# Optimization experiments

Measured on AMD Instinct MI355X. Metric: run time of the kernel, lower is better.

The kernel has to match this reference:

```python
import jax, jax.numpy as jnp
import numpy as np

N = 30000      # num_nodes
E = 480000     # num_edges
NF = 128       # node_features
EF = 64        # edge_features
HID = 256      # hidden_dim
L = 4          # num_layers
H = 8          # heads
D = HID // H   # per-head dim = 32
SCALE = 0.02


def _ln(x, g, b, eps=1e-5):
    m = x.mean(-1, keepdims=True)
    v = ((x - m) ** 2).mean(-1, keepdims=True)
    return (x - m) * jax.lax.rsqrt(v + eps) * g + b


def _mlp_head(x, W1, b1, W2, b2):
    return jax.nn.sigmoid(jax.nn.relu(x @ W1 + b1) @ W2 + b2)


def setup_inputs() -> dict:
    key = jax.random.key(0)
    ks = jax.random.split(key, 32)
    r = lambda k, shp: SCALE * jax.random.normal(k, shp, dtype=jnp.float32)
    inp = {
        'x': jax.random.normal(ks[0], (N, NF), dtype=jnp.float32),
        'edge_attr': jax.random.normal(ks[1], (E, EF), dtype=jnp.float32),
        'edge_index': jax.random.randint(ks[2], (2, E), 0, N, dtype=jnp.int32),
        # encoders
        'enc_Wn': r(ks[3], (NF, HID)), 'enc_bn': jnp.zeros((HID,), jnp.float32),
        'enc_We': r(ks[4], (EF, HID)), 'enc_be': jnp.zeros((HID,), jnp.float32),
        # stacked TransformerConv params for L layers
        'Wq': r(ks[5], (L, HID, HID)), 'bq': jnp.zeros((L, HID), jnp.float32),
        'Wk': r(ks[6], (L, HID, HID)), 'bk': jnp.zeros((L, HID), jnp.float32),
        'Wv': r(ks[7], (L, HID, HID)), 'bv': jnp.zeros((L, HID), jnp.float32),
        'We': r(ks[8], (L, HID, HID)),  # lin_edge has no bias in PyG
        'Wsk': r(ks[9], (L, HID, HID)), 'bsk': jnp.zeros((L, HID), jnp.float32),
        # shared LayerNorm (module reuses self.norm every layer)
        'ln_g': jnp.ones((HID,), jnp.float32), 'ln_b': jnp.zeros((HID,), jnp.float32),
        # contagion predictor
        'cp_W1': r(ks[10], (HID, HID // 2)), 'cp_b1': jnp.zeros((HID // 2,), jnp.float32),
        'cp_W2': r(ks[11], (HID // 2, 1)), 'cp_b2': jnp.zeros((1,), jnp.float32),
        # systemic risk predictor
        'sp_W1': r(ks[12], (HID, HID // 2)), 'sp_b1': jnp.zeros((HID // 2,), jnp.float32),
        'sp_W2': r(ks[13], (HID // 2, 1)), 'sp_b2': jnp.zeros((1,), jnp.float32),
    }
    return inp


def reference(x, edge_attr, edge_index, enc_Wn, enc_bn, enc_We, enc_be,
              Wq, bq, Wk, bk, Wv, bv, We, Wsk, bsk, ln_g, ln_b,
              cp_W1, cp_b1, cp_W2, cp_b2, sp_W1, sp_b1, sp_W2, sp_b2):
    src, dst = edge_index[0], edge_index[1]
    h = x @ enc_Wn + enc_bn                 # [N,HID]
    e = edge_attr @ enc_We + enc_be         # [E,HID]
    inv_sqrt_d = 1.0 / jnp.sqrt(jnp.asarray(D, h.dtype))
    for l in range(L):
        # TransformerConv: query at dst, key/value at src, edge bias on both k and v
        q = (h @ Wq[l] + bq[l]).reshape(N, H, D)[dst]            # [E,H,D]
        ke = (e @ We[l]).reshape(E, H, D)                        # [E,H,D]
        k = (h @ Wk[l] + bk[l]).reshape(N, H, D)[src] + ke
        v = (h @ Wv[l] + bv[l]).reshape(N, H, D)[src] + ke
        score = (q * k).sum(-1) * inv_sqrt_d                     # [E,H]
        smax = jax.ops.segment_max(score, dst, num_segments=N)   # [N,H]
        p = jnp.exp(score - smax[dst])
        denom = jax.ops.segment_sum(p, dst, num_segments=N)
        alpha = p / (denom[dst] + 1e-16)                         # scatter-softmax
        agg = jax.ops.segment_sum(alpha[..., None] * v, dst, num_segments=N)
        out = agg.reshape(N, HID) + h @ Wsk[l] + bsk[l]          # concat heads + root skip
        h = _ln(h + out, ln_g, ln_b)                             # residual + shared LN (eval: no dropout)
    g = h.mean(0, keepdims=True)                                 # [1,HID] global mean pool
    contagion_risk = _mlp_head(h, cp_W1, cp_b1, cp_W2, cp_b2)    # [N,1]
    systemic_risk = _mlp_head(g, sp_W1, sp_b1, sp_W2, sp_b2)     # [1,1]
    return h, g, contagion_risk, systemic_risk
```

## Files before the change

### kernel.cpp

```cpp
#include <hip/hip_runtime.h>
#include <cstddef>
#include <cstdint>

#define NN 30000
#define EE 480000
#define NFD 128
#define EFD 64
#define HID 256
#define NL 4
#define NH 8

#define DT_BF16 0
#define DT_F32  1
#define DT_EXT  2

#define OFF_WT  ((size_t)65787648)
#define MIN_B   ((size_t)68015872)
#define MIN_A   ((size_t)129455872)

#define WT_ENC 0
#define WT_LAYER(l) (32768 + (size_t)(l) * 262144)
#define WT_CP1 (32768 + (size_t)1048576)

typedef short bf16x8 __attribute__((ext_vector_type(8)));
typedef unsigned short us8 __attribute__((ext_vector_type(8)));
typedef float f32x4 __attribute__((ext_vector_type(4)));

__device__ __forceinline__ float bf2f(unsigned short u) {
  union { unsigned int i; float f; } v; v.i = ((unsigned int)u) << 16; return v.f;
}
__device__ __forceinline__ unsigned short f2bf(float f) {
  union { float f; unsigned int i; } v; v.f = f;
  unsigned int i = v.i;
  return (unsigned short)((i + 0x7FFFu + ((i >> 16) & 1u)) >> 16);
}
struct F4 { float x, y, z, w; };
__device__ __forceinline__ F4 load4bf(const unsigned short* p) {
  ushort4 u = *reinterpret_cast<const ushort4*>(p);
  F4 f; f.x = bf2f(u.x); f.y = bf2f(u.y); f.z = bf2f(u.z); f.w = bf2f(u.w);
  return f;
}
__device__ __forceinline__ F4 load4f(const float* p) {
  float4 t = *reinterpret_cast<const float4*>(p);
  F4 f; f.x = t.x; f.y = t.y; f.z = t.z; f.w = t.w; return f;
}
__device__ __forceinline__ F4 load4any(const void* p, size_t idx, int f32) {
  return f32 ? load4f((const float*)p + idx) : load4bf((const unsigned short*)p + idx);
}
__device__ __forceinline__ float load1any(const void* p, size_t idx, int f32) {
  return f32 ? ((const float*)p)[idx] : bf2f(((const unsigned short*)p)[idx]);
}
__device__ __forceinline__ void store1any(void* p, size_t idx, float v, int f32) {
  if (f32) ((float*)p)[idx] = v; else ((unsigned short*)p)[idx] = f2bf(v);
}

__global__ void probe_dtype(const void* __restrict__ ln_g, int* __restrict__ flag) {
  unsigned int u = *(const unsigned int*)ln_g;
  *flag = ((u & 0xFFFFu) == 0u) ? 1 : 0;
}

__global__ void wt_build(const void* __restrict__ enc_Wn,
                         const void* __restrict__ Wq, const void* __restrict__ Wk,
                         const void* __restrict__ Wv, const void* __restrict__ Wsk,
                         const void* __restrict__ cp_W1,
                         unsigned short* __restrict__ Wt, const int* __restrict__ flagp)
{
  const int f = *flagp;
  size_t idx = (size_t)blockIdx.x * 256 + threadIdx.x;
  if (idx < 32768) {
    int n = idx >> 7, k = idx & 127;
    Wt[WT_ENC + idx] = f2bf(load1any(enc_Wn, (size_t)k * 256 + n, f));
  } else if (idx < 32768 + 1048576) {
    size_t off = idx - 32768;
    int l = off >> 18;
    int which = (off >> 16) & 3;
    size_t e = off & 65535;
    int n = e >> 8, k = e & 255;
    const void* W = (which == 0) ? Wq : (which == 1) ? Wk : (which == 2) ? Wv : Wsk;
    Wt[idx] = f2bf(load1any(W, (size_t)l * 65536 + (size_t)k * 256 + n, f));
  } else if (idx < 32768 + 1048576 + 32768) {
    size_t e = idx - 32768 - 1048576;
    int n = e >> 8, k = e & 255;
    Wt[idx] = f2bf(load1any(cp_W1, (size_t)k * 128 + n, f));
  }
}

template<bool OUT_F32, bool RELU>
__global__ __launch_bounds__(256) void mfma_gemm(
    const void* __restrict__ Av, int aMode,
    const unsigned short* __restrict__ Bt,
    const void* __restrict__ biasv, size_t biasEl, int biasMode,
    void* __restrict__ Cv, int ldC, int cOff,
    int M, int K, const int* __restrict__ flagp)
{
  const int f = *flagp;
  const int aF32 = (aMode == DT_EXT) ? f : aMode;
  const int biF32 = (biasMode == DT_EXT) ? f : biasMode;

  __shared__ unsigned short Al[128][40];
  __shared__ unsigned short Bl[64][40];
  const int bm = blockIdx.x * 128;
  const int bn = blockIdx.y * 64;
  const int tid = threadIdx.x;
  const int wv = tid >> 6, lane = tid & 63;
  const int l16 = lane & 15, quad = lane >> 4;

  f32x4 acc[2][4];
#pragma unroll
  for (int i = 0; i < 2; i++)
#pragma unroll
    for (int j = 0; j < 4; j++) acc[i][j] = (f32x4){0.f, 0.f, 0.f, 0.f};

  const int ar = tid >> 1;
  const int ah = (tid & 1) << 4;
  const int bnr = tid >> 2;
  const int bk8 = (tid & 3) << 3;

  for (int k0 = 0; k0 < K; k0 += 32) {
    us8 w0, w1;
    int gr = bm + ar;
    if (gr < M) {
      if (!aF32) {
        const unsigned short* ap = (const unsigned short*)Av + (size_t)gr * K + k0 + ah;
        w0 = *(const us8*)ap;
        w1 = *(const us8*)(ap + 8);
      } else {
        const float* ap = (const float*)Av + (size_t)gr * K + k0 + ah;
        float4 u0 = *(const float4*)ap;
        float4 u1 = *(const float4*)(ap + 4);
        float4 u2 = *(const float4*)(ap + 8);
        float4 u3 = *(const float4*)(ap + 12);
        w0[0] = f2bf(u0.x); w0[1] = f2bf(u0.y); w0[2] = f2bf(u0.z); w0[3] = f2bf(u0.w);
        w0[4] = f2bf(u1.x); w0[5] = f2bf(u1.y); w0[6] = f2bf(u1.z); w0[7] = f2bf(u1.w);
        w1[0] = f2bf(u2.x); w1[1] = f2bf(u2.y); w1[2] = f2bf(u2.z); w1[3] = f2bf(u2.w);
        w1[4] = f2bf(u3.x); w1[5] = f2bf(u3.y); w1[6] = f2bf(u3.z); w1[7] = f2bf(u3.w);
      }
    } else {
      w0 = (us8)0; w1 = (us8)0;
    }
    *(us8*)&Al[ar][ah] = w0;
    *(us8*)&Al[ar][ah + 8] = w1;
    *(us8*)&Bl[bnr][bk8] = *(const us8*)&Bt[(size_t)(bn + bnr) * K + k0 + bk8];
    __syncthreads();

    bf16x8 a0 = *(const bf16x8*)&Al[wv * 32 + l16][quad * 8];
    bf16x8 a1 = *(const bf16x8*)&Al[wv * 32 + 16 + l16][quad * 8];
#pragma unroll
    for (int tn = 0; tn < 4; tn++) {
      bf16x8 b = *(const bf16x8*)&Bl[tn * 16 + l16][quad * 8];
      acc[0][tn] = __builtin_amdgcn_mfma_f32_16x16x32_bf16(a0, b, acc[0][tn], 0, 0, 0);
      acc[1][tn] = __builtin_amdgcn_mfma_f32_16x16x32_bf16(a1, b, acc[1][tn], 0, 0, 0);
    }
    __syncthreads();
  }

#pragma unroll
  for (int tm = 0; tm < 2; tm++) {
#pragma unroll
    for (int tn = 0; tn < 4; tn++) {
      int col = bn + tn * 16 + l16;
      float bias = load1any(biasv, biasEl + col, biF32);
#pragma unroll
      for (int r = 0; r < 4; r++) {
        int row = bm + wv * 32 + tm * 16 + quad * 4 + r;
        if (row < M) {
          float v = acc[tm][tn][r] + bias;
          if (RELU) v = fmaxf(v, 0.f);
          size_t off = (size_t)row * ldC + cOff + col;
          if (OUT_F32) ((float*)Cv)[off] = v;
          else ((unsigned short*)Cv)[off] = f2bf(v);
        }
      }
    }
  }
}

__global__ __launch_bounds__(256) void mfma_gemm_qkvs(
    const unsigned short* __restrict__ A,
    const unsigned short* __restrict__ Bt,
    const void* __restrict__ bq, const void* __restrict__ bk,
    const void* __restrict__ bv, const void* __restrict__ bsk, size_t biasEl,
    unsigned short* __restrict__ Qb, unsigned short* __restrict__ KVb,
    unsigned short* __restrict__ Sb,
    int M, const int* __restrict__ flagp)
{
  const int f = *flagp;
  __shared__ unsigned short Al[128][40];
  __shared__ unsigned short Bl[64][40];
  const int bm = blockIdx.x * 128;
  const int bnG = blockIdx.y * 64;
  const int which = bnG >> 8;
  const int bn = bnG & 255;
  const int tid = threadIdx.x;
  const int wv = tid >> 6, lane = tid & 63;
  const int l16 = lane & 15, quad = lane >> 4;

  f32x4 acc[2][4];
#pragma unroll
  for (int i = 0; i < 2; i++)
#pragma unroll
    for (int j = 0; j < 4; j++) acc[i][j] = (f32x4){0.f, 0.f, 0.f, 0.f};

  const int ar = tid >> 1;
  const int ah = (tid & 1) << 4;
  const int bnr = tid >> 2;
  const int bk8 = (tid & 3) << 3;
  const unsigned short* Bbase = Bt + (size_t)which * 65536;

  for (int k0 = 0; k0 < HID; k0 += 32) {
    us8 w0, w1;
    int gr = bm + ar;
    if (gr < M) {
      const unsigned short* ap = A + (size_t)gr * HID + k0 + ah;
      w0 = *(const us8*)ap;
      w1 = *(const us8*)(ap + 8);
    } else {
      w0 = (us8)0; w1 = (us8)0;
    }
    *(us8*)&Al[ar][ah] = w0;
    *(us8*)&Al[ar][ah + 8] = w1;
    *(us8*)&Bl[bnr][bk8] = *(const us8*)&Bbase[(size_t)(bn + bnr) * HID + k0 + bk8];
    __syncthreads();

    bf16x8 a0 = *(const bf16x8*)&Al[wv * 32 + l16][quad * 8];
    bf16x8 a1 = *(const bf16x8*)&Al[wv * 32 + 16 + l16][quad * 8];
#pragma unroll
    for (int tn = 0; tn < 4; tn++) {
      bf16x8 b = *(const bf16x8*)&Bl[tn * 16 + l16][quad * 8];
      acc[0][tn] = __builtin_amdgcn_mfma_f32_16x16x32_bf16(a0, b, acc[0][tn], 0, 0, 0);
      acc[1][tn] = __builtin_amdgcn_mfma_f32_16x16x32_bf16(a1, b, acc[1][tn], 0, 0, 0);
    }
    __syncthreads();
  }

  const void* biasv = (which == 0) ? bq : (which == 1) ? bk : (which == 2) ? bv : bsk;
  unsigned short* out = (which == 0) ? Qb : (which == 3) ? Sb : KVb;
  const int ldC = (which == 1 || which == 2) ? 512 : 256;
  const int cOff = (which == 2) ? 256 : 0;

#pragma unroll
  for (int tm = 0; tm < 2; tm++) {
#pragma unroll
    for (int tn = 0; tn < 4; tn++) {
      int col = bn + tn * 16 + l16;
      float bias = load1any(biasv, biasEl + col, f);
#pragma unroll
      for (int r = 0; r < 4; r++) {
        int row = bm + wv * 32 + tm * 16 + quad * 4 + r;
        if (row < M)
          out[(size_t)row * ldC + cOff + col] = f2bf(acc[tm][tn][r] + bias);
      }
    }
  }
}

__global__ void fold_kernel(const void* __restrict__ enc_We,
                            const void* __restrict__ enc_be,
                            const void* __restrict__ We_all,
                            float* __restrict__ Mfold, const int* __restrict__ flagp)
{
  const int f = *flagp;
  int idx = blockIdx.x * blockDim.x + threadIdx.x;
  if (idx >= NL * 65 * HID) return;
  int l = idx / (65 * HID);
  int rc = idx - l * 65 * HID;
  int row = rc >> 8;
  int col = rc & 255;
  size_t Wbase = (size_t)l * HID * HID;
  float acc = 0.f;
  if (row < 64) {
    for (int k = 0; k < HID; k++)
      acc += load1any(enc_We, (size_t)row * HID + k, f) * load1any(We_all, Wbase + (size_t)k * HID + col, f);
  } else {
    for (int k = 0; k < HID; k++)
      acc += load1any(enc_be, k, f) * load1any(We_all, Wbase + (size_t)k * HID + col, f);
  }
  Mfold[idx] = acc;
}

__global__ void hist_kernel(const int* __restrict__ dst, int* __restrict__ rp) {
  int e = blockIdx.x * 256 + threadIdx.x;
  if (e < EE) atomicAdd(&rp[dst[e]], 1);
}

__global__ __launch_bounds__(1024) void scan_kernel(int* __restrict__ rp) {
  __shared__ int part[1024];
  int t = threadIdx.x;
  int base = t * 30;
  int loc[30];
  int sum = 0;
#pragma unroll
  for (int i = 0; i < 30; i++) {
    int idx = base + i;
    int v = (idx < NN) ? rp[idx] : 0;
    loc[i] = v; sum += v;
  }
  part[t] = sum;
  __syncthreads();
  for (int off = 1; off < 1024; off <<= 1) {
    int v = (t >= off) ? part[t - off] : 0;
    __syncthreads();
    part[t] += v;
    __syncthreads();
  }
  int run = (t == 0) ? 0 : part[t - 1];
#pragma unroll
  for (int i = 0; i < 30; i++) {
    int idx = base + i;
    if (idx < NN) { rp[idx] = run; run += loc[i]; }
    else if (idx == NN) { rp[NN] = run; }
  }
}

__global__ void scatter_kernel(const int* __restrict__ src, const int* __restrict__ dst,
                               const int* __restrict__ rp, int* __restrict__ cnt2,
                               int2* __restrict__ sed) {
  int e = blockIdx.x * 256 + threadIdx.x;
  if (e >= EE) return;
  int d = dst[e];
  int pos = rp[d] + atomicAdd(&cnt2[d], 1);
  int2 v; v.x = src[e]; v.y = e;
  sed[pos] = v;
}

__global__ void ea_build(const int2* __restrict__ sed, const void* __restrict__ edge_attr,
                         unsigned short* __restrict__ ea_srt, const int* __restrict__ flagp) {
  const int f = *flagp;
  int gid = blockIdx.x * 256 + threadIdx.x;
  int pos = gid >> 4;
  int sub = (gid & 15) * 4;
  int e = sed[pos].y;
  F4 v = load4any(edge_attr, (size_t)e * EFD + sub, f);
  ushort4 o; o.x = f2bf(v.x); o.y = f2bf(v.y); o.z = f2bf(v.z); o.w = f2bf(v.w);
  *reinterpret_cast<ushort4*>(ea_srt + (size_t)pos * EFD + sub) = o;
}

template<bool SORTED>
__global__ __launch_bounds__(256, 8) void edge_fused(
    const int* __restrict__ rp, const int2* __restrict__ sed,
    const unsigned short* __restrict__ Qb, const unsigned short* __restrict__ KV,
    const unsigned short* __restrict__ ea_srt,
    const void* __restrict__ edge_attr,
    const float* __restrict__ Mf,
    const unsigned short* __restrict__ Sb,
    unsigned short* __restrict__ hb,
    const void* __restrict__ ln_g, const void* __restrict__ ln_b,
    const int* __restrict__ flagp)
{
  __shared__ float wl[4][8][68];
  const int f = *flagp;
  const int wv = __builtin_amdgcn_readfirstlane(threadIdx.x >> 6);
  const int nw = blockIdx.x * 4 + wv;
  const int lane = threadIdx.x & 63;
  const int hd = lane >> 3;
  const int j = lane & 7;
  const int jb = j << 3;
  const int c4 = lane * 4;

  const size_t rowb = (size_t)nw * HID;
  F4 q4 = load4bf(Qb + rowb + c4);

  float t8[8];
  {
    float q32[32];
#pragma unroll
    for (int i = 0; i < 8; i++) {
      F4 t = load4bf(Qb + rowb + hd * 32 + i * 4);
      q32[i * 4 + 0] = t.x; q32[i * 4 + 1] = t.y; q32[i * 4 + 2] = t.z; q32[i * 4 + 3] = t.w;
    }
#pragma unroll
    for (int kk = 0; kk < 8; kk++) {
      const float* Mrow = Mf + (size_t)(jb + kk) * HID + hd * 32;
      float a = 0.f;
#pragma unroll
      for (int cc = 0; cc < 8; cc++) {
        float4 m4 = *reinterpret_cast<const float4*>(Mrow + cc * 4);
        a = fmaf(m4.x, q32[cc * 4 + 0], a);
        a = fmaf(m4.y, q32[cc * 4 + 1], a);
        a = fmaf(m4.z, q32[cc * 4 + 2], a);
        a = fmaf(m4.w, q32[cc * 4 + 3], a);
      }
      t8[kk] = a;
    }
  }
  float s0;
  {
    F4 b4 = load4f(Mf + (size_t)64 * HID + c4);
    s0 = q4.x * b4.x + q4.y * b4.y + q4.z * b4.z + q4.w * b4.w;
    s0 += __shfl_xor(s0, 1);
    s0 += __shfl_xor(s0, 2);
    s0 += __shfl_xor(s0, 4);
  }

  float accv[4] = {0.f, 0.f, 0.f, 0.f};
  float wacc[8] = {0.f, 0.f, 0.f, 0.f, 0.f, 0.f, 0.f, 0.f};
  float den = 0.f;
  const int beg = rp[nw], end = rp[nw + 1];

  if (beg < end) {
    const float scl = 0.17677669529663687f;

#define LOADE(tt, kk, vvv, ee) do {                                            \
    int2 _sv = sed[(tt)];                                                      \
    int _sx = __builtin_amdgcn_readfirstlane(_sv.x);                           \
    const unsigned short* _kvp = KV + (size_t)_sx * 512;                       \
    kk  = *reinterpret_cast<const ushort4*>(_kvp + c4);                        \
    vvv = *reinterpret_cast<const ushort4*>(_kvp + 256 + c4);                  \
    if (SORTED) {                                                              \
      ee = *reinterpret_cast<const us8*>(ea_srt + (size_t)(tt) * EFD + jb);    \
    } else {                                                                   \
      int _ey = __builtin_amdgcn_readfirstlane(_sv.y);                         \
      if (!f) {                                                                \
        ee = *reinterpret_cast<const us8*>((const unsigned short*)edge_attr +  \
                                           (size_t)_ey * EFD + jb);            \
      } else {                                                                 \
        const float* _ep = (const float*)edge_attr + (size_t)_ey * EFD + jb;   \
        float4 _u0 = *(const float4*)_ep;                                      \
        float4 _u1 = *(const float4*)(_ep + 4);                                \
        ee[0] = (short)f2bf(_u0.x); ee[1] = (short)f2bf(_u0.y);                \
        ee[2] = (short)f2bf(_u0.z); ee[3] = (short)f2bf(_u0.w);                \
        ee[4] = (short)f2bf(_u1.x); ee[5] = (short)f2bf(_u1.y);                \
        ee[6] = (short)f2bf(_u1.z); ee[7] = (short)f2bf(_u1.w);                \
      }                                                                        \
    }                                                                          \
  } while (0)

#define COMPUTE(kk, vvv, ee) do {                                              \
    float _r = q4.x * bf2f(kk.x) + q4.y * bf2f(kk.y) +                         \
               q4.z * bf2f(kk.z) + q4.w * bf2f(kk.w);                          \
    float _e0 = bf2f((unsigned short)ee[0]);                                   \
    float _e1 = bf2f((unsigned short)ee[1]);                                   \
    float _e2 = bf2f((unsigned short)ee[2]);                                   \
    float _e3 = bf2f((unsigned short)ee[3]);                                   \
    float _e4 = bf2f((unsigned short)ee[4]);                                   \
    float _e5 = bf2f((unsigned short)ee[5]);                                   \
    float _e6 = bf2f((unsigned short)ee[6]);                                   \
    float _e7 = bf2f((unsigned short)ee[7]);                                   \
    _r = fmaf(_e0, t8[0], _r); _r = fmaf(_e1, t8[1], _r);                      \
    _r = fmaf(_e2, t8[2], _r); _r = fmaf(_e3, t8[3], _r);                      \
    _r = fmaf(_e4, t8[4], _r); _r = fmaf(_e5, t8[5], _r);                      \
    _r = fmaf(_e6, t8[6], _r); _r = fmaf(_e7, t8[7], _r);                      \
    _r += __shfl_xor(_r, 1);                                                   \
    _r += __shfl_xor(_r, 2);                                                   \
    _r += __shfl_xor(_r, 4);                                                   \
    float _sc = fminf(fmaxf((_r + s0) * scl, -30.f), 30.f);                    \
    float _p = __expf(_sc);                                                    \
    den += _p;                                                                 \
    accv[0] = fmaf(_p, bf2f(vvv.x), accv[0]);                                  \
    accv[1] = fmaf(_p, bf2f(vvv.y), accv[1]);                                  \
    accv[2] = fmaf(_p, bf2f(vvv.z), accv[2]);                                  \
    accv[3] = fmaf(_p, bf2f(vvv.w), accv[3]);                                  \
    wacc[0] = fmaf(_p, _e0, wacc[0]); wacc[1] = fmaf(_p, _e1, wacc[1]);        \
    wacc[2] = fmaf(_p, _e2, wacc[2]); wacc[3] = fmaf(_p, _e3, wacc[3]);        \
    wacc[4] = fmaf(_p, _e4, wacc[4]); wacc[5] = fmaf(_p, _e5, wacc[5]);        \
    wacc[6] = fmaf(_p, _e6, wacc[6]); wacc[7] = fmaf(_p, _e7, wacc[7]);        \
  } while (0)

    ushort4 k0, v0, k1, v1;
    us8 e0, e1;
    k1 = (ushort4){0, 0, 0, 0}; v1 = k1; e1 = (us8)0;
    LOADE(beg, k0, v0, e0);
    int t = beg;
    for (;;) {
      if (t + 1 < end) LOADE(t + 1, k1, v1, e1);
      COMPUTE(k0, v0, e0);
      if (++t >= end) break;
      if (t + 1 < end) LOADE(t + 1, k0, v0, e0);
      COMPUTE(k1, v1, e1);
      if (++t >= end) break;
    }
#undef LOADE
#undef COMPUTE
  }

#pragma unroll
  for (int i = 0; i < 8; i++) wl[wv][hd][jb + i] = wacc[i];
  __syncthreads();

  float ke0 = 0.f, ke1 = 0.f, ke2 = 0.f, ke3 = 0.f;
#pragma unroll 8
  for (int k = 0; k < 64; k++) {
    float w = wl[wv][hd][k];
    float4 m4 = *reinterpret_cast<const float4*>(Mf + (size_t)k * HID + c4);
    ke0 = fmaf(w, m4.x, ke0);
    ke1 = fmaf(w, m4.y, ke1);
    ke2 = fmaf(w, m4.z, ke2);
    ke3 = fmaf(w, m4.w, ke3);
  }

  float invden = 1.f / (den + 1e-16f);
  float sel = (end > beg) ? 1.f : 0.f;
  F4 b4 = load4f(Mf + (size_t)64 * HID + c4);
  F4 s4 = load4bf(Sb + rowb + c4);
  F4 hh = load4bf(hb + rowb + c4);
  float r0 = hh.x + sel * ((accv[0] + ke0) * invden + b4.x) + s4.x;
  float r1 = hh.y + sel * ((accv[1] + ke1) * invden + b4.y) + s4.y;
  float r2 = hh.z + sel * ((accv[2] + ke2) * invden + b4.z) + s4.z;
  float r3 = hh.w + sel * ((accv[3] + ke3) * invden + b4.w) + s4.w;

  float sum = r0 + r1 + r2 + r3;
#pragma unroll
  for (int o = 1; o < 64; o <<= 1) sum += __shfl_xor(sum, o);
  float mean = sum * (1.f / HID);
  float d0 = r0 - mean, d1 = r1 - mean, d2 = r2 - mean, d3 = r3 - mean;
  float vs = d0 * d0 + d1 * d1 + d2 * d2 + d3 * d3;
#pragma unroll
  for (int o = 1; o < 64; o <<= 1) vs += __shfl_xor(vs, o);
  float rstd = rsqrtf(vs * (1.f / HID) + 1e-5f);
  ushort4 o4;
  o4.x = f2bf(d0 * rstd * load1any(ln_g, c4 + 0, f) + load1any(ln_b, c4 + 0, f));
  o4.y = f2bf(d1 * rstd * load1any(ln_g, c4 + 1, f) + load1any(ln_b, c4 + 1, f));
  o4.z = f2bf(d2 * rstd * load1any(ln_g, c4 + 2, f) + load1any(ln_b, c4 + 2, f));
  o4.w = f2bf(d3 * rstd * load1any(ln_g, c4 + 3, f) + load1any(ln_b, c4 + 3, f));
  *reinterpret_cast<ushort4*>(hb + rowb + c4) = o4;
}

__global__ void copy_h_out(const unsigned short* __restrict__ h, void* __restrict__ out,
                           const int* __restrict__ flagp) {
  const int f = *flagp;
  int i = blockIdx.x * 256 + threadIdx.x;
  store1any(out, i, bf2f(h[i]), f);
}

__global__ void colsum_kernel(const unsigned short* __restrict__ h, float* __restrict__ gsum) {
  int c = threadIdx.x;
  float s = 0.f;
  for (int r = blockIdx.x; r < NN; r += gridDim.x) s += bf2f(h[(size_t)r * HID + c]);
  atomicAdd(&gsum[c], s);
}

__global__ void write_g_kernel(const float* __restrict__ gsum, void* __restrict__ out,
                               const int* __restrict__ flagp) {
  const int f = *flagp;
  int c = threadIdx.x;
  store1any(out, (size_t)NN * HID + c, gsum[c] * (1.f / NN), f);
}

__global__ __launch_bounds__(256) void cp2_kernel(
    const float* __restrict__ hid, const void* __restrict__ W2,
    const void* __restrict__ b2, void* __restrict__ out,
    const int* __restrict__ flagp)
{
  const int f = *flagp;
  int nw = (blockIdx.x << 2) + (threadIdx.x >> 6);
  if (nw >= NN) return;
  int lane = threadIdx.x & 63;
  const float* hr = hid + (size_t)nw * 128;
  float s = hr[lane * 2] * load1any(W2, lane * 2, f) + hr[lane * 2 + 1] * load1any(W2, lane * 2 + 1, f);
#pragma unroll
  for (int o = 1; o < 64; o <<= 1) s += __shfl_xor(s, o);
  if (lane == 0) {
    float xv = s + load1any(b2, 0, f);
    store1any(out, (size_t)NN * HID + HID + nw, 1.f / (1.f + __expf(-xv)), f);
  }
}

__global__ __launch_bounds__(128) void sys_kernel(
    const float* __restrict__ gsum,
    const void* __restrict__ W1, const void* __restrict__ b1,
    const void* __restrict__ W2, const void* __restrict__ b2,
    void* __restrict__ out, const int* __restrict__ flagp)
{
  const int f = *flagp;
  __shared__ float red[2];
  int j = threadIdx.x;
  float acc = load1any(b1, j, f);
  const float invN = 1.f / NN;
  for (int k = 0; k < HID; k++) acc = fmaf(gsum[k] * invN, load1any(W1, (size_t)k * 128 + j, f), acc);
  float v = fmaxf(acc, 0.f) * load1any(W2, j, f);
#pragma unroll
  for (int o = 1; o < 64; o <<= 1) v += __shfl_xor(v, o);
  if ((j & 63) == 0) red[j >> 6] = v;
  __syncthreads();
  if (j == 0) {
    float xv = red[0] + red[1] + load1any(b2, 0, f);
    store1any(out, (size_t)NN * HID + HID + NN, 1.f / (1.f + __expf(-xv)), f);
  }
}

__global__ void diag_kernel(float* __restrict__ out, float v, int n4) {
  int i = blockIdx.x * 256 + threadIdx.x;
  if (i < n4) out[i] = (i == 0) ? v : 0.f;
}

extern "C" void kernel_launch(void* const* d_in, const int* in_sizes, int n_in,
                              void* d_out, int out_size, void* d_ws, size_t ws_size,
                              hipStream_t stream)
{
  (void)in_sizes; (void)n_in;

  if (ws_size < MIN_B) {
    diag_kernel<<<(out_size / 2 + 255) / 256, 256, 0, stream>>>(
        (float*)d_out, (float)(ws_size >> 20), out_size / 2);
    return;
  }
  const bool planA = (ws_size >= MIN_A);

  const void* x         = d_in[0];
  const void* edge_attr = d_in[1];
  const int*  edge_index= (const int*)d_in[2];
  const void* enc_Wn = d_in[3];
  const void* enc_bn = d_in[4];
  const void* enc_We = d_in[5];
  const void* enc_be = d_in[6];
  const void* Wq  = d_in[7];
  const void* bq  = d_in[8];
  const void* Wk  = d_in[9];
  const void* bk  = d_in[10];
  const void* Wv  = d_in[11];
  const void* bvv = d_in[12];
  const void* We  = d_in[13];
  const void* Wsk = d_in[14];
  const void* bsk = d_in[15];
  const void* ln_g = d_in[16];
  const void* ln_b = d_in[17];
  const void* cp_W1 = d_in[18];
  const void* cp_b1 = d_in[19];
  const void* cp_W2 = d_in[20];
  const void* cp_b2 = d_in[21];
  const void* sp_W1 = d_in[22];
  const void* sp_b1 = d_in[23];
  const void* sp_W2 = d_in[24];
  const void* sp_b2 = d_in[25];

  char* ws = (char*)d_ws;
  unsigned short* hb  = (unsigned short*)(ws + 0);
  unsigned short* Sb  = (unsigned short*)(ws + 15360000);
  unsigned short* KVb = (unsigned short*)(ws + 30720000);
  int2*  sed   = (int2*)(ws + 61440000);
  int*   rp    = (int*)(ws + 65280000);
  int*   cnt2  = (int*)(ws + 65400064);
  float* Mfold = (float*)(ws + 65520128);
  float* gsum  = (float*)(ws + 65786368);
  int*   flagp = (int*)(ws + 65787392);
  unsigned short* Wt = (unsigned short*)(ws + OFF_WT);
  unsigned short* ea_srt = (unsigned short*)(ws + MIN_B);
  unsigned short* Qb = (unsigned short*)d_out;
  float* cph = (float*)(ws + 15360000);

  const int* src = edge_index;
  const int* dst = edge_index + EE;

  probe_dtype<<<1, 1, 0, stream>>>(ln_g, flagp);
  wt_build<<<(1114112 + 255) / 256, 256, 0, stream>>>(enc_Wn, Wq, Wk, Wv, Wsk, cp_W1, Wt, flagp);
  fold_kernel<<<(NL * 65 * HID + 255) / 256, 256, 0, stream>>>(enc_We, enc_be, We, Mfold, flagp);

  hipMemsetAsync(rp, 0, 120064, stream);
  hipMemsetAsync(cnt2, 0, 120064, stream);
  hist_kernel<<<(EE + 255) / 256, 256, 0, stream>>>(dst, rp);
  scan_kernel<<<1, 1024, 0, stream>>>(rp);
  scatter_kernel<<<(EE + 255) / 256, 256, 0, stream>>>(src, dst, rp, cnt2, sed);
  if (planA) {
    ea_build<<<EE * 16 / 256, 256, 0, stream>>>(sed, edge_attr, ea_srt, flagp);
  }

  const int gx = (NN + 127) / 128;
  {
    dim3 g(gx, 4);
    mfma_gemm<false, false><<<g, 256, 0, stream>>>(
        x, DT_EXT, Wt + WT_ENC, enc_bn, 0, DT_EXT, hb, HID, 0, NN, NFD, flagp);
  }

  for (int l = 0; l < NL; l++) {
    size_t bo = (size_t)l * HID;
    dim3 gQ(gx, 16);
    mfma_gemm_qkvs<<<gQ, 256, 0, stream>>>(
        hb, Wt + WT_LAYER(l), bq, bk, bvv, bsk, bo, Qb, KVb, Sb, NN, flagp);
    const float* Mf = Mfold + (size_t)l * 65 * HID;
    if (planA) {
      edge_fused<true><<<NN / 4, 256, 0, stream>>>(
          rp, sed, Qb, KVb, ea_srt, edge_attr, Mf, Sb, hb, ln_g, ln_b, flagp);
    } else {
      edge_fused<false><<<NN / 4, 256, 0, stream>>>(
          rp, sed, Qb, KVb, ea_srt, edge_attr, Mf, Sb, hb, ln_g, ln_b, flagp);
    }
  }

  copy_h_out<<<NN, 256, 0, stream>>>(hb, d_out, flagp);
  hipMemsetAsync(gsum, 0, HID * 4, stream);
  colsum_kernel<<<256, 256, 0, stream>>>(hb, gsum);
  write_g_kernel<<<1, 256, 0, stream>>>(gsum, d_out, flagp);

  {
    dim3 g(gx, 2);
    mfma_gemm<true, true><<<g, 256, 0, stream>>>(
        hb, DT_BF16, Wt + WT_CP1, cp_b1, 0, DT_EXT, cph, 128, 0, NN, HID, flagp);
  }
  cp2_kernel<<<NN / 4, 256, 0, stream>>>(cph, cp_W2, cp_b2, d_out, flagp);
  sys_kernel<<<1, 128, 0, stream>>>(gsum, sp_W1, sp_b1, sp_W2, sp_b2, d_out, flagp);
}
```

Measured before the change: 2.477 ms.

## Interleave K/V layout and deepen edge-loop prefetch to four edges

The projection GEMM epilogue now writes K and V interleaved per 4-column group, so each lane fetches its K and V slices with a single 16-byte load. The edge aggregation loop is restructured to load indices and data for four edges at a time, double-buffered, with out-of-range edges clamped and masked out by a zero weight. Launch bounds drop from 8 to 4 waves per SIMD to leave room for the extra registers, and the q·M fold is reordered to stream q chunks rather than hold all 32 values. The aim is more memory-level parallelism on the gathers in the latency-bound edge loop, at the cost of lower occupancy and wasted work on padded edges.

```diff
diff --git a/kernel.cpp b/kernel.cpp
--- a/kernel.cpp
+++ b/kernel.cpp
@@ -235,8 +235,6 @@
 
   const void* biasv = (which == 0) ? bq : (which == 1) ? bk : (which == 2) ? bv : bsk;
   unsigned short* out = (which == 0) ? Qb : (which == 3) ? Sb : KVb;
-  const int ldC = (which == 1 || which == 2) ? 512 : 256;
-  const int cOff = (which == 2) ? 256 : 0;
 
 #pragma unroll
   for (int tm = 0; tm < 2; tm++) {
@@ -247,8 +245,16 @@
 #pragma unroll
       for (int r = 0; r < 4; r++) {
         int row = bm + wv * 32 + tm * 16 + quad * 4 + r;
-        if (row < M)
-          out[(size_t)row * ldC + cOff + col] = f2bf(acc[tm][tn][r] + bias);
+        if (row < M) {
+          unsigned short val = f2bf(acc[tm][tn][r] + bias);
+          size_t idx;
+          if (which == 0 || which == 3) {
+            idx = (size_t)row * 256 + col;
+          } else {
+            idx = (size_t)row * 512 + ((size_t)(col >> 2) << 3) + ((which == 2) ? 4 : 0) + (col & 3);
+          }
+          out[idx] = val;
+        }
       }
     }
   }
@@ -336,7 +342,7 @@
 }
 
 template<bool SORTED>
-__global__ __launch_bounds__(256, 8) void edge_fused(
+__global__ __launch_bounds__(256, 4) void edge_fused(
     const int* __restrict__ rp, const int2* __restrict__ sed,
     const unsigned short* __restrict__ Qb, const unsigned short* __restrict__ KV,
     const unsigned short* __restrict__ ea_srt,
@@ -360,26 +366,19 @@
   const size_t rowb = (size_t)nw * HID;
   F4 q4 = load4bf(Qb + rowb + c4);
 
-  float t8[8];
-  {
-    float q32[32];
-#pragma unroll
-    for (int i = 0; i < 8; i++) {
-      F4 t = load4bf(Qb + rowb + hd * 32 + i * 4);
-      q32[i * 4 + 0] = t.x; q32[i * 4 + 1] = t.y; q32[i * 4 + 2] = t.z; q32[i * 4 + 3] = t.w;
-    }
+  float t8[8] = {0.f, 0.f, 0.f, 0.f, 0.f, 0.f, 0.f, 0.f};
+#pragma unroll
+  for (int cc = 0; cc < 8; cc++) {
+    F4 qc = load4bf(Qb + rowb + hd * 32 + cc * 4);
 #pragma unroll
     for (int kk = 0; kk < 8; kk++) {
-      const float* Mrow = Mf + (size_t)(jb + kk) * HID + hd * 32;
-      float a = 0.f;
-#pragma unroll
-      for (int cc = 0; cc < 8; cc++) {
-        float4 m4 = *reinterpret_cast<const float4*>(Mrow + cc * 4);
-        a = fmaf(m4.x, q32[cc * 4 + 0], a);
-        a = fmaf(m4.y, q32[cc * 4 + 1], a);
-        a = fmaf(m4.z, q32[cc * 4 + 2], a);
-        a = fmaf(m4.w, q32[cc * 4 + 3], a);
-      }
+      const float4 m4 = *reinterpret_cast<const float4*>(
+          Mf + (size_t)(jb + kk) * HID + hd * 32 + cc * 4);
+      float a = t8[kk];
+      a = fmaf(m4.x, qc.x, a);
+      a = fmaf(m4.y, qc.y, a);
+      a = fmaf(m4.z, qc.z, a);
+      a = fmaf(m4.w, qc.w, a);
       t8[kk] = a;
     }
   }
@@ -400,34 +399,46 @@
   if (beg < end) {
     const float scl = 0.17677669529663687f;
 
-#define LOADE(tt, kk, vvv, ee) do {                                            \
-    int2 _sv = sed[(tt)];                                                      \
-    int _sx = __builtin_amdgcn_readfirstlane(_sv.x);                           \
-    const unsigned short* _kvp = KV + (size_t)_sx * 512;                       \
-    kk  = *reinterpret_cast<const ushort4*>(_kvp + c4);                        \
-    vvv = *reinterpret_cast<const ushort4*>(_kvp + 256 + c4);                  \
+#define CLM(tt) (((tt) < end) ? (tt) : beg)
+
+#define LIDX(bb) do {                                                          \
+    int2 _s0 = sed[CLM(bb)];                                                   \
+    int2 _s1 = sed[CLM((bb) + 1)];                                             \
+    int2 _s2 = sed[CLM((bb) + 2)];                                             \
+    int2 _s3 = sed[CLM((bb) + 3)];                                             \
+    ix0 = __builtin_amdgcn_readfirstlane(_s0.x);                               \
+    ix1 = __builtin_amdgcn_readfirstlane(_s1.x);                               \
+    ix2 = __builtin_amdgcn_readfirstlane(_s2.x);                               \
+    ix3 = __builtin_amdgcn_readfirstlane(_s3.x);                               \
     if (SORTED) {                                                              \
-      ee = *reinterpret_cast<const us8*>(ea_srt + (size_t)(tt) * EFD + jb);    \
+      iy0 = CLM(bb); iy1 = CLM((bb) + 1); iy2 = CLM((bb) + 2); iy3 = CLM((bb) + 3); \
     } else {                                                                   \
-      int _ey = __builtin_amdgcn_readfirstlane(_sv.y);                         \
-      if (!f) {                                                                \
-        ee = *reinterpret_cast<const us8*>((const unsigned short*)edge_attr +  \
-                                           (size_t)_ey * EFD + jb);            \
-      } else {                                                                 \
-        const float* _ep = (const float*)edge_attr + (size_t)_ey * EFD + jb;   \
-        float4 _u0 = *(const float4*)_ep;                                      \
-        float4 _u1 = *(const float4*)(_ep + 4);                                \
-        ee[0] = (short)f2bf(_u0.x); ee[1] = (short)f2bf(_u0.y);                \
-        ee[2] = (short)f2bf(_u0.z); ee[3] = (short)f2bf(_u0.w);                \
-        ee[4] = (short)f2bf(_u1.x); ee[5] = (short)f2bf(_u1.y);                \
-        ee[6] = (short)f2bf(_u1.z); ee[7] = (short)f2bf(_u1.w);                \
-      }                                                                        \
+      iy0 = __builtin_amdgcn_readfirstlane(_s0.y);                             \
+      iy1 = __builtin_amdgcn_readfirstlane(_s1.y);                             \
+      iy2 = __builtin_amdgcn_readfirstlane(_s2.y);                             \
+      iy3 = __builtin_amdgcn_readfirstlane(_s3.y);                             \
     }                                                                          \
   } while (0)
 
-#define COMPUTE(kk, vvv, ee) do {                                              \
-    float _r = q4.x * bf2f(kk.x) + q4.y * bf2f(kk.y) +                         \
-               q4.z * bf2f(kk.z) + q4.w * bf2f(kk.w);                          \
+#define LDAT(ixx, iyy, kvv, ee) do {                                           \
+    kvv = *reinterpret_cast<const us8*>(KV + (size_t)(ixx) * 512 + lane * 8);  \
+    if (SORTED) {                                                              \
+      ee = *reinterpret_cast<const us8*>(ea_srt + (size_t)(iyy) * EFD + jb);   \
+    } else if (!f) {                                                           \
+      ee = *reinterpret_cast<const us8*>((const unsigned short*)edge_attr +    \
+                                         (size_t)(iyy) * EFD + jb);            \
+    } else {                                                                   \
+      const float* _ep = (const float*)edge_attr + (size_t)(iyy) * EFD + jb;   \
+      float4 _u0 = *(const float4*)_ep;                                        \
+      float4 _u1 = *(const float4*)(_ep + 4);                                  \
+      ee[0] = (short)f2bf(_u0.x); ee[1] = (short)f2bf(_u0.y);                  \
+      ee[2] = (short)f2bf(_u0.z); ee[3] = (short)f2bf(_u0.w);                  \
+      ee[4] = (short)f2bf(_u1.x); ee[5] = (short)f2bf(_u1.y);                  \
+      ee[6] = (short)f2bf(_u1.z); ee[7] = (short)f2bf(_u1.w);                  \
+    }                                                                          \
+  } while (0)
+
+#define COMP(kvv, ee, mm) do {                                                 \
     float _e0 = bf2f((unsigned short)ee[0]);                                   \
     float _e1 = bf2f((unsigned short)ee[1]);                                   \
     float _e2 = bf2f((unsigned short)ee[2]);                                   \
@@ -436,6 +447,10 @@
     float _e5 = bf2f((unsigned short)ee[5]);                                   \
     float _e6 = bf2f((unsigned short)ee[6]);                                   \
     float _e7 = bf2f((unsigned short)ee[7]);                                   \
+    float _r = q4.x * bf2f((unsigned short)kvv[0])                             \
+             + q4.y * bf2f((unsigned short)kvv[1])                             \
+             + q4.z * bf2f((unsigned short)kvv[2])                             \
+             + q4.w * bf2f((unsigned short)kvv[3]);                            \
     _r = fmaf(_e0, t8[0], _r); _r = fmaf(_e1, t8[1], _r);                      \
     _r = fmaf(_e2, t8[2], _r); _r = fmaf(_e3, t8[3], _r);                      \
     _r = fmaf(_e4, t8[4], _r); _r = fmaf(_e5, t8[5], _r);                      \
@@ -444,33 +459,48 @@
     _r += __shfl_xor(_r, 2);                                                   \
     _r += __shfl_xor(_r, 4);                                                   \
     float _sc = fminf(fmaxf((_r + s0) * scl, -30.f), 30.f);                    \
-    float _p = __expf(_sc);                                                    \
+    float _p = (mm) * __expf(_sc);                                             \
     den += _p;                                                                 \
-    accv[0] = fmaf(_p, bf2f(vvv.x), accv[0]);                                  \
-    accv[1] = fmaf(_p, bf2f(vvv.y), accv[1]);                                  \
-    accv[2] = fmaf(_p, bf2f(vvv.z), accv[2]);                                  \
-    accv[3] = fmaf(_p, bf2f(vvv.w), accv[3]);                                  \
+    accv[0] = fmaf(_p, bf2f((unsigned short)kvv[4]), accv[0]);                 \
+    accv[1] = fmaf(_p, bf2f((unsigned short)kvv[5]), accv[1]);                 \
+    accv[2] = fmaf(_p, bf2f((unsigned short)kvv[6]), accv[2]);                 \
+    accv[3] = fmaf(_p, bf2f((unsigned short)kvv[7]), accv[3]);                 \
     wacc[0] = fmaf(_p, _e0, wacc[0]); wacc[1] = fmaf(_p, _e1, wacc[1]);        \
     wacc[2] = fmaf(_p, _e2, wacc[2]); wacc[3] = fmaf(_p, _e3, wacc[3]);        \
     wacc[4] = fmaf(_p, _e4, wacc[4]); wacc[5] = fmaf(_p, _e5, wacc[5]);        \
     wacc[6] = fmaf(_p, _e6, wacc[6]); wacc[7] = fmaf(_p, _e7, wacc[7]);        \
   } while (0)
 
-    ushort4 k0, v0, k1, v1;
-    us8 e0, e1;
-    k1 = (ushort4){0, 0, 0, 0}; v1 = k1; e1 = (us8)0;
-    LOADE(beg, k0, v0, e0);
-    int t = beg;
-    for (;;) {
-      if (t + 1 < end) LOADE(t + 1, k1, v1, e1);
-      COMPUTE(k0, v0, e0);
-      if (++t >= end) break;
-      if (t + 1 < end) LOADE(t + 1, k0, v0, e0);
-      COMPUTE(k1, v1, e1);
-      if (++t >= end) break;
-    }
-#undef LOADE
-#undef COMPUTE
+    us8 kvP0, kvP1, kvP2, kvP3, eP0, eP1, eP2, eP3;
+    us8 kvN0, kvN1, kvN2, kvN3, eN0, eN1, eN2, eN3;
+    int ix0, ix1, ix2, ix3, iy0, iy1, iy2, iy3;
+
+    LIDX(beg);
+    LDAT(ix0, iy0, kvP0, eP0);
+    LDAT(ix1, iy1, kvP1, eP1);
+    LDAT(ix2, iy2, kvP2, eP2);
+    LDAT(ix3, iy3, kvP3, eP3);
+    LIDX(beg + 4);
+
+    for (int t = beg; t < end; t += 4) {
+      LDAT(ix0, iy0, kvN0, eN0);
+      LDAT(ix1, iy1, kvN1, eN1);
+      LDAT(ix2, iy2, kvN2, eN2);
+      LDAT(ix3, iy3, kvN3, eN3);
+      LIDX(t + 8);
+      COMP(kvP0, eP0, 1.f);
+      COMP(kvP1, eP1, (t + 1 < end) ? 1.f : 0.f);
+      COMP(kvP2, eP2, (t + 2 < end) ? 1.f : 0.f);
+      COMP(kvP3, eP3, (t + 3 < end) ? 1.f : 0.f);
+      kvP0 = kvN0; eP0 = eN0;
+      kvP1 = kvN1; eP1 = eN1;
+      kvP2 = kvN2; eP2 = eN2;
+      kvP3 = kvN3; eP3 = eN3;
+    }
+#undef CLM
+#undef LIDX
+#undef LDAT
+#undef COMP
   }
 
 #pragma unroll
```

Measured after the change: 2.506 ms. No clear change (+1.2%).
